# Kernel optimization log

Hardware: AMD Instinct MI355X
Metric: run time of the kernel (lower is better)

The kernel has to match this reference:

```python
import jax, jax.numpy as jnp
import numpy as np

B, S, D, H = 2, 2048, 1024, 16
HD = D // H  # head_dim = 64


def setup_inputs() -> dict:
    key = jax.random.key(0)
    ks = jax.random.split(key, 8)
    scale = 0.02
    return {
        "hidden_states": jax.random.normal(ks[0], (B, S, D), dtype=jnp.float32),
        "attn_mask": jnp.zeros((B, 1, 1, S), dtype=jnp.float32),  # additive mask
        "Wq": jax.random.normal(ks[1], (D, D), dtype=jnp.float32) * scale,
        "bq": jnp.zeros((D,), dtype=jnp.float32),
        "Wk": jax.random.normal(ks[2], (D, D), dtype=jnp.float32) * scale,
        "bk": jnp.zeros((D,), dtype=jnp.float32),
        "Wv": jax.random.normal(ks[3], (D, D), dtype=jnp.float32) * scale,
        "bv": jnp.zeros((D,), dtype=jnp.float32),
    }


def reference(hidden_states, attn_mask, Wq, bq, Wk, bk, Wv, bv):
    # QKV projections: nn.Linear(dim, dim) -> x @ W.T + b
    def proj(x, W, b):
        y = jnp.einsum("bsd,ed->bse", x, W) + b
        # split heads: [B, S, D] -> [B, H, S, HD]
        return y.reshape(B, S, H, HD).transpose(0, 2, 1, 3)

    q = proj(hidden_states, Wq, bq)
    k = proj(hidden_states, Wk, bk)
    v = proj(hidden_states, Wv, bv)

    # scaled dot-product scores + additive mask (hack_torch_trace(scores, mask))
    scores = jnp.einsum("bhqd,bhkd->bhqk", q, k) / jnp.sqrt(jnp.float32(HD))
    scores = scores + attn_mask  # broadcast [B,1,1,S]
    probs = jax.nn.softmax(scores, axis=-1)  # attn dropout = identity (eval)

    ctx = jnp.einsum("bhqk,bhkd->bhqd", probs, v)
    # merge heads: [B, H, S, HD] -> [B, S, D]
    attn_outputs = ctx.transpose(0, 2, 1, 3).reshape(B, S, D)
    return attn_outputs
```

## Files before the change

kernel.cpp:

```cpp
#include <hip/hip_runtime.h>
#include <hip/hip_bf16.h>
#include <math.h>


typedef __bf16 bf16_t;
typedef __attribute__((ext_vector_type(8))) __bf16 bf16x8;
typedef __attribute__((ext_vector_type(4))) __bf16 bf16x4;
typedef __attribute__((ext_vector_type(4))) float f32x4;

#define B_  2
#define S_  2048
#define D_  1024
#define H_  16
#define HD_ 64
#define M_  (B_ * S_)
#define K_  D_
#define NT_ (S_ / 64)
#define LOG2E 1.44269504f
#define CS_Q (0.125f * LOG2E)

__device__ __forceinline__ f32x4 mfma16x16x32(bf16x8 a, bf16x8 b, f32x4 c) {
    return __builtin_amdgcn_mfma_f32_16x16x32_bf16(a, b, c, 0, 0, 0);
}

__device__ __forceinline__ void gload_lds16(const bf16_t* g, bf16_t* l) {
    __builtin_amdgcn_global_load_lds(
        (const __attribute__((address_space(1))) void*)g,
        (__attribute__((address_space(3))) void*)l,
        16, 0, 0);
}

__global__ void cvt_all(const float* __restrict__ hs, const float* __restrict__ wq,
                        const float* __restrict__ wk, const float* __restrict__ wv,
                        const float* __restrict__ mask,
                        bf16_t* __restrict__ Xb, bf16_t* __restrict__ Wb3,
                        float* __restrict__ mk2) {
    const int i = blockIdx.x * blockDim.x + threadIdx.x;
    if (i >= 1835008) {
        const int off = i - 1835008;
        if (off < 1024) {
            float4 v = ((const float4*)mask)[off];
            v.x = v.x * LOG2E - 8.0f; v.y = v.y * LOG2E - 8.0f;
            v.z = v.z * LOG2E - 8.0f; v.w = v.w * LOG2E - 8.0f;
            ((float4*)mk2)[off] = v;
        }
        return;
    }
    const float* src; bf16_t* dst; int off;
    if (i < 1048576)      { src = hs; dst = Xb;            off = i; }
    else if (i < 1310720) { src = wq; dst = Wb3;           off = i - 1048576; }
    else if (i < 1572864) { src = wk; dst = Wb3 + 1048576; off = i - 1310720; }
    else                  { src = wv; dst = Wb3 + 2097152; off = i - 1572864; }
    float4 v = ((const float4*)src)[off];
    bf16x4 o;
    o[0] = (bf16_t)v.x; o[1] = (bf16_t)v.y;
    o[2] = (bf16_t)v.z; o[3] = (bf16_t)v.w;
    ((bf16x4*)dst)[off] = o;
}

__global__ __launch_bounds__(256, 2)
void gemm_qkv(const bf16_t* __restrict__ Xb, const bf16_t* __restrict__ Wb3,
              const float* __restrict__ bq, const float* __restrict__ bk,
              const float* __restrict__ bv,
              bf16_t* __restrict__ Qo, bf16_t* __restrict__ Ko,
              bf16_t* __restrict__ Vf) {
    __shared__ bf16_t smem[2][8192];
    const int z = blockIdx.z;
    const bf16_t* Wb = Wb3 + (size_t)z * (D_ * K_);
    const float* bias = (z == 0) ? bq : (z == 1) ? bk : bv;

    const int tid  = threadIdx.x;
    const int lane = tid & 63;
    const int w    = tid >> 6;
    const int wr   = w >> 1, wc = w & 1;
    const int m0   = blockIdx.y * 128;
    const int n0   = blockIdx.x * 128;

    f32x4 acc[4][4];
    const f32x4 fzero = {0.f, 0.f, 0.f, 0.f};
#pragma unroll
    for (int i = 0; i < 4; i++)
#pragma unroll
        for (int j = 0; j < 4; j++) acc[i][j] = fzero;

    const int koff = (lane >> 4) * 8;

    auto stage = [&](int k0, int buf) {
#pragma unroll
        for (int i = 0; i < 4; i++) {
            const int chunk  = w * 4 + i;
            const int byteoff = chunk * 1024 + lane * 16;
            bf16_t* ldst = &smem[buf][chunk * 512];
            const bf16_t* gsrc;
            if (byteoff < 8192) {
                int row = byteoff >> 6;
                int col = (byteoff & 63) >> 1;
                gsrc = Xb + (size_t)(m0 + row) * K_ + k0 + col;
            } else {
                int bo  = byteoff - 8192;
                int row = bo >> 6;
                int col = (bo & 63) >> 1;
                gsrc = Wb + (size_t)(n0 + row) * K_ + k0 + col;
            }
            gload_lds16(gsrc, ldst);
        }
    };

    stage(0, 0);
    __syncthreads();

    for (int kk = 0; kk < K_ / 32; ++kk) {
        const int cur = kk & 1;
        if (kk + 1 < K_ / 32) stage((kk + 1) * 32, cur ^ 1);

        bf16x8 af[4], bfr[4];
#pragma unroll
        for (int m = 0; m < 4; m++) {
            int row = wr * 64 + m * 16 + (lane & 15);
            af[m] = *(const bf16x8*)&smem[cur][row * 32 + koff];
        }
#pragma unroll
        for (int n = 0; n < 4; n++) {
            int row = wc * 64 + n * 16 + (lane & 15);
            bfr[n] = *(const bf16x8*)&smem[cur][4096 + row * 32 + koff];
        }
#pragma unroll
        for (int m = 0; m < 4; m++)
#pragma unroll
            for (int n = 0; n < 4; n++)
                acc[m][n] = mfma16x16x32(af[m], bfr[n], acc[m][n]);

        __syncthreads();
    }

#pragma unroll
    for (int m = 0; m < 4; m++) {
        const int gm    = m0 + wr * 64 + m * 16 + ((lane >> 4) << 2);
        const int bidx  = gm >> 11;
        const int sbase = gm & 2047;
#pragma unroll
        for (int n = 0; n < 4; n++) {
            const int gn = n0 + wc * 64 + n * 16 + (lane & 15);
            const int h  = gn >> 6, hd = gn & 63;
            const float bias_v = bias[gn];
            const size_t bh = (size_t)bidx * H_ + h;
            if (z == 2) {
                const int t   = sbase >> 6, k0i = sbase & 63;
                const int nb  = k0i >> 4, kgf = (k0i >> 2) & 3;
                const int db  = hd >> 4,  lqf = hd & 15;
                bf16x4 pack;
#pragma unroll
                for (int j = 0; j < 4; j++)
                    pack[j] = (bf16_t)(acc[m][n][j] + bias_v);
                bf16_t* dst = Vf + ((bh * 32 + t) * 4 + db) * 1024 +
                    (kgf * 16 + lqf) * 16 + nb * 4;
                *(bf16x4*)dst = pack;
            } else if (z == 0) {
#pragma unroll
                for (int j = 0; j < 4; j++) {
                    float y = (acc[m][n][j] + bias_v) * CS_Q;
                    Qo[(bh * S_ + sbase + j) * HD_ + hd] = (bf16_t)y;
                }
            } else {
#pragma unroll
                for (int j = 0; j < 4; j++) {
                    float y = acc[m][n][j] + bias_v;
                    Ko[(bh * S_ + sbase + j) * HD_ + hd] = (bf16_t)y;
                }
            }
        }
    }
}

__global__ __launch_bounds__(256, 2)
void attn_fwd(const bf16_t* __restrict__ Qb, const bf16_t* __restrict__ Kb,
              const bf16_t* __restrict__ Vf, const float* __restrict__ mk2b,
              float* __restrict__ out) {
    const int flat = blockIdx.x;
    const int xcd  = flat & 7;
    const int idx  = flat >> 3;
    const int bh   = xcd * 4 + (idx >> 4);
    const int qt   = idx & 15;
    const int b    = bh >> 4;
    const int h    = bh & 15;

    const int tid  = threadIdx.x, lane = tid & 63, w = tid >> 6;

    const bf16_t* Qh = Qb + (size_t)bh * S_ * HD_;
    const bf16_t* Kh = Kb + (size_t)bh * S_ * HD_;
    const bf16_t* Vh = Vf + (size_t)bh * 32 * 4096;
    const float*  mk = mk2b + (size_t)b * S_;

    __shared__ char ShBuf[16384];

    const int lq   = lane & 15;
    const int kg   = lane >> 4;
    const int koff = kg * 8;
    const int rsub = lane >> 3;
    const int csl8 = (lane & 7) * 8;

    auto stageK = [&](int kv0, int buf) {
        bf16_t* base = (bf16_t*)(ShBuf + buf * 8192);
#pragma unroll
        for (int i = 0; i < 2; i++) {
            const int c = w * 2 + i;
            bf16_t* ldst = base + c * 512;
            const int cel = csl8 ^ (rsub * 8);
            const bf16_t* gsrc = Kh + (size_t)(kv0 + c * 8 + rsub) * HD_ + cel;
            gload_lds16(gsrc, ldst);
        }
    };

    const int qbase = qt * 128 + w * 32;
    bf16x8 qf0[2], qf1[2];
#pragma unroll
    for (int s = 0; s < 2; s++) {
        const bf16_t* qr = Qh + (size_t)(qbase + s * 16 + lq) * HD_;
        qf0[s] = *(const bf16x8*)(qr + koff);
        qf1[s] = *(const bf16x8*)(qr + 32 + koff);
    }

    bf16x8 ones;
#pragma unroll
    for (int e = 0; e < 8; e++) ones[e] = (bf16_t)1.0f;

    const f32x4 fzero = {0.f, 0.f, 0.f, 0.f};
    f32x4 of[2][4];
    f32x4 of_l[2];
#pragma unroll
    for (int s = 0; s < 2; s++) {
        of_l[s] = fzero;
#pragma unroll
        for (int i = 0; i < 4; i++) of[s][i] = fzero;
    }

    const int rdsw = (lq & 7) << 4;

    stageK(0, 0);
    __syncthreads();

    for (int t = 0; t < NT_; ++t) {
        const int cur = t & 1;
        const int kv0 = t * 64;

        f32x4 mC[4];
#pragma unroll
        for (int nb = 0; nb < 4; nb++)
            mC[nb] = *(const f32x4*)&mk[kv0 + nb * 16 + kg * 4];

        const bf16_t* Vt_ = Vh + (size_t)t * 4096;
        bf16x8 va[4], vb[4];
#pragma unroll
        for (int db = 0; db < 4; db++) {
            const bf16_t* vp = Vt_ + db * 1024 + lane * 16;
            va[db] = *(const bf16x8*)(vp);
            vb[db] = *(const bf16x8*)(vp + 8);
        }

        if (t + 1 < NT_) stageK((t + 1) * 64, cur ^ 1);

        const char* KB = ShBuf + cur * 8192;

        bf16x8 kf0[4], kf1[4];
#pragma unroll
        for (int nb = 0; nb < 4; nb++) {
            const char* kr = KB + (nb * 16 + lq) * 128;
            kf0[nb] = *(const bf16x8*)(kr + ((kg * 16) ^ rdsw));
            kf1[nb] = *(const bf16x8*)(kr + ((64 + kg * 16) ^ rdsw));
        }

#pragma unroll
        for (int s = 0; s < 2; s++) {
            f32x4 sc[4];
#pragma unroll
            for (int nb = 0; nb < 4; nb++) {
                f32x4 tacc = mC[nb];
                tacc = mfma16x16x32(kf0[nb], qf0[s], tacc);
                tacc = mfma16x16x32(kf1[nb], qf1[s], tacc);
                sc[nb] = tacc;
            }

            bf16x8 pa0, pa1;
#pragma unroll
            for (int nb = 0; nb < 4; nb++)
#pragma unroll
                for (int j = 0; j < 4; j++) {
                    float p = exp2f(sc[nb][j]);
                    const int e = (nb & 1) * 4 + j;
                    if (nb < 2) pa0[e] = (bf16_t)p; else pa1[e] = (bf16_t)p;
                }

#pragma unroll
            for (int db = 0; db < 4; db++) {
                of[s][db] = mfma16x16x32(pa0, va[db], of[s][db]);
                of[s][db] = mfma16x16x32(pa1, vb[db], of[s][db]);
            }
            of_l[s] = mfma16x16x32(pa0, ones, of_l[s]);
            of_l[s] = mfma16x16x32(pa1, ones, of_l[s]);
        }

        __syncthreads();
    }

#pragma unroll
    for (int s = 0; s < 2; s++) {
        float inv[4];
#pragma unroll
        for (int j = 0; j < 4; j++) inv[j] = 1.0f / of_l[s][j];
#pragma unroll
        for (int db = 0; db < 4; db++) {
            const int d = h * HD_ + db * 16 + lq;
#pragma unroll
            for (int j = 0; j < 4; j++) {
                const int row = qbase + s * 16 + kg * 4 + j;
                out[((size_t)b * S_ + row) * D_ + d] = of[s][db][j] * inv[j];
            }
        }
    }
}

extern "C" void kernel_launch(void* const* d_in, const int* in_sizes, int n_in,
                              void* d_out, int out_size, void* d_ws, size_t ws_size,
                              hipStream_t stream) {
    const float* hs   = (const float*)d_in[0];
    const float* mask = (const float*)d_in[1];
    const float* Wq   = (const float*)d_in[2];
    const float* bq   = (const float*)d_in[3];
    const float* Wk   = (const float*)d_in[4];
    const float* bk   = (const float*)d_in[5];
    const float* Wv   = (const float*)d_in[6];
    const float* bv   = (const float*)d_in[7];
    float* out = (float*)d_out;

    char* ws = (char*)d_ws;
    bf16_t* Xb  = (bf16_t*)(ws);
    bf16_t* Wb3 = (bf16_t*)(ws + 8388608);
    bf16_t* Qb  = (bf16_t*)(ws + 14680064);
    bf16_t* Kb  = (bf16_t*)(ws + 23068672);
    bf16_t* Vfr = (bf16_t*)(ws + 31457280);
    float*  mk2 = (float*)(ws + 39845888);

    cvt_all<<<7172, 256, 0, stream>>>(hs, Wq, Wk, Wv, mask, Xb, Wb3, mk2);

    dim3 ggrid(D_ / 128, M_ / 128, 3);
    gemm_qkv<<<ggrid, 256, 0, stream>>>(Xb, Wb3, bq, bk, bv, Qb, Kb, Vfr);

    attn_fwd<<<512, 256, 0, stream>>>(Qb, Kb, Vfr, mk2, out);
}
```

Before: 99.52 us.

## Fold additive mask into V and row-sum weights as multiplicative factors

```diff
diff --git a/kernel.cpp b/kernel.cpp
--- a/kernel.cpp
+++ b/kernel.cpp
@@ -34,15 +34,24 @@
                         const float* __restrict__ wk, const float* __restrict__ wv,
                         const float* __restrict__ mask,
                         bf16_t* __restrict__ Xb, bf16_t* __restrict__ Wb3,
-                        float* __restrict__ mk2) {
+                        float* __restrict__ wfp, bf16_t* __restrict__ wfb) {
     const int i = blockIdx.x * blockDim.x + threadIdx.x;
     if (i >= 1835008) {
         const int off = i - 1835008;
         if (off < 1024) {
             float4 v = ((const float4*)mask)[off];
-            v.x = v.x * LOG2E - 8.0f; v.y = v.y * LOG2E - 8.0f;
-            v.z = v.z * LOG2E - 8.0f; v.w = v.w * LOG2E - 8.0f;
-            ((float4*)mk2)[off] = v;
+            float4 w4;
+            w4.x = exp2f(v.x * LOG2E); w4.y = exp2f(v.y * LOG2E);
+            w4.z = exp2f(v.z * LOG2E); w4.w = exp2f(v.w * LOG2E);
+            ((float4*)wfp)[off] = w4;
+            const int k4 = off * 4;
+            const int bb = k4 >> 11, k = k4 & 2047;
+            const int t  = k >> 6,  kt = k & 63;
+            const int nb = kt >> 4, kgf = (kt >> 2) & 3;
+            bf16x4 wb4;
+            wb4[0] = (bf16_t)w4.x; wb4[1] = (bf16_t)w4.y;
+            wb4[2] = (bf16_t)w4.z; wb4[3] = (bf16_t)w4.w;
+            *(bf16x4*)&wfb[(((size_t)bb * 32 + t) * 4 + kgf) * 16 + nb * 4] = wb4;
         }
         return;
     }
@@ -62,6 +71,7 @@
 void gemm_qkv(const bf16_t* __restrict__ Xb, const bf16_t* __restrict__ Wb3,
               const float* __restrict__ bq, const float* __restrict__ bk,
               const float* __restrict__ bv,
+              const float* __restrict__ wfp,
               bf16_t* __restrict__ Qo, bf16_t* __restrict__ Ko,
               bf16_t* __restrict__ Vf) {
     __shared__ bf16_t smem[2][8192];
@@ -148,10 +158,12 @@
                 const int t   = sbase >> 6, k0i = sbase & 63;
                 const int nb  = k0i >> 4, kgf = (k0i >> 2) & 3;
                 const int db  = hd >> 4,  lqf = hd & 15;
+                const float4 w4 = *(const float4*)&wfp[bidx * S_ + sbase];
                 bf16x4 pack;
-#pragma unroll
-                for (int j = 0; j < 4; j++)
-                    pack[j] = (bf16_t)(acc[m][n][j] + bias_v);
+                pack[0] = (bf16_t)((acc[m][n][0] + bias_v) * w4.x);
+                pack[1] = (bf16_t)((acc[m][n][1] + bias_v) * w4.y);
+                pack[2] = (bf16_t)((acc[m][n][2] + bias_v) * w4.z);
+                pack[3] = (bf16_t)((acc[m][n][3] + bias_v) * w4.w);
                 bf16_t* dst = Vf + ((bh * 32 + t) * 4 + db) * 1024 +
                     (kgf * 16 + lqf) * 16 + nb * 4;
                 *(bf16x4*)dst = pack;
@@ -174,7 +186,7 @@
 
 __global__ __launch_bounds__(256, 2)
 void attn_fwd(const bf16_t* __restrict__ Qb, const bf16_t* __restrict__ Kb,
-              const bf16_t* __restrict__ Vf, const float* __restrict__ mk2b,
+              const bf16_t* __restrict__ Vf, const bf16_t* __restrict__ Wfb,
               float* __restrict__ out) {
     const int flat = blockIdx.x;
     const int xcd  = flat & 7;
@@ -189,7 +201,7 @@
     const bf16_t* Qh = Qb + (size_t)bh * S_ * HD_;
     const bf16_t* Kh = Kb + (size_t)bh * S_ * HD_;
     const bf16_t* Vh = Vf + (size_t)bh * 32 * 4096;
-    const float*  mk = mk2b + (size_t)b * S_;
+    const bf16_t* Wh = Wfb + (size_t)b * 32 * 64;
 
     __shared__ char ShBuf[16384];
 
@@ -220,10 +232,6 @@
         qf1[s] = *(const bf16x8*)(qr + 32 + koff);
     }
 
-    bf16x8 ones;
-#pragma unroll
-    for (int e = 0; e < 8; e++) ones[e] = (bf16_t)1.0f;
-
     const f32x4 fzero = {0.f, 0.f, 0.f, 0.f};
     f32x4 of[2][4];
     f32x4 of_l[2];
@@ -241,12 +249,10 @@
 
     for (int t = 0; t < NT_; ++t) {
         const int cur = t & 1;
-        const int kv0 = t * 64;
-
-        f32x4 mC[4];
-#pragma unroll
-        for (int nb = 0; nb < 4; nb++)
-            mC[nb] = *(const f32x4*)&mk[kv0 + nb * 16 + kg * 4];
+
+        const bf16_t* wp = Wh + (size_t)t * 64 + kg * 16;
+        bf16x8 wf0 = *(const bf16x8*)(wp);
+        bf16x8 wf1 = *(const bf16x8*)(wp + 8);
 
         const bf16_t* Vt_ = Vh + (size_t)t * 4096;
         bf16x8 va[4], vb[4];
@@ -274,7 +280,7 @@
             f32x4 sc[4];
 #pragma unroll
             for (int nb = 0; nb < 4; nb++) {
-                f32x4 tacc = mC[nb];
+                f32x4 tacc = fzero;
                 tacc = mfma16x16x32(kf0[nb], qf0[s], tacc);
                 tacc = mfma16x16x32(kf1[nb], qf1[s], tacc);
                 sc[nb] = tacc;
@@ -295,8 +301,8 @@
                 of[s][db] = mfma16x16x32(pa0, va[db], of[s][db]);
                 of[s][db] = mfma16x16x32(pa1, vb[db], of[s][db]);
             }
-            of_l[s] = mfma16x16x32(pa0, ones, of_l[s]);
-            of_l[s] = mfma16x16x32(pa1, ones, of_l[s]);
+            of_l[s] = mfma16x16x32(pa0, wf0, of_l[s]);
+            of_l[s] = mfma16x16x32(pa1, wf1, of_l[s]);
         }
 
         __syncthreads();
@@ -338,12 +344,13 @@
     bf16_t* Qb  = (bf16_t*)(ws + 14680064);
     bf16_t* Kb  = (bf16_t*)(ws + 23068672);
     bf16_t* Vfr = (bf16_t*)(ws + 31457280);
-    float*  mk2 = (float*)(ws + 39845888);
-
-    cvt_all<<<7172, 256, 0, stream>>>(hs, Wq, Wk, Wv, mask, Xb, Wb3, mk2);
+    float*  wfp = (float*)(ws + 39845888);
+    bf16_t* wfb = (bf16_t*)(ws + 39862272);
+
+    cvt_all<<<7172, 256, 0, stream>>>(hs, Wq, Wk, Wv, mask, Xb, Wb3, wfp, wfb);
 
     dim3 ggrid(D_ / 128, M_ / 128, 3);
-    gemm_qkv<<<ggrid, 256, 0, stream>>>(Xb, Wb3, bq, bk, bv, Qb, Kb, Vfr);
-
-    attn_fwd<<<512, 256, 0, stream>>>(Qb, Kb, Vfr, mk2, out);
-}
+    gemm_qkv<<<ggrid, 256, 0, stream>>>(Xb, Wb3, bq, bk, bv, wfp, Qb, Kb, Vfr);
+
+    attn_fwd<<<512, 256, 0, stream>>>(Qb, Kb, Vfr, wfb, out);
+}
```

New measurement: 99.32 us. Within noise of the previous version (-0.2%).
